# Performance work log

Measured on AMD Instinct MI355X. Metric: run time of the kernel, lower is better.

Reference implementation:

```python
import jax, jax.numpy as jnp
import numpy as np

HEAD_DIM = 64
AGGR = 4  # attn_aggr_ratio
BN_EPS = 1e-5


def _conv1x1(x, W, b=None):
    # x: [N, Cin, L], W: [Cout, Cin] -> [N, Cout, L]
    y = jnp.einsum('ncl,oc->nol', x, W)
    if b is not None:
        y = y + b[None, :, None]
    return y


def _bn(x, gamma, beta, mean, var):
    # BatchNorm1d, eval mode (running stats). x: [N, C, L]
    inv = gamma * jax.lax.rsqrt(var + BN_EPS)
    return x * inv[None, :, None] + (beta - mean * inv)[None, :, None]


def setup_inputs() -> dict:
    key = jax.random.key(0)
    ks = jax.random.split(key, 8)
    N, C, L = 4, 256, 4096
    s = 1.0 / np.sqrt(C)
    inp = {
        'x': jax.random.normal(ks[0], (N, C, L), jnp.float32),
        'Wq': jax.random.normal(ks[1], (C, C), jnp.float32) * s,
        'bq': jnp.zeros((C,), jnp.float32),
        'Wk': jax.random.normal(ks[2], (C, C), jnp.float32) * s,
        'bk': jnp.zeros((C,), jnp.float32),
        'Wv': jax.random.normal(ks[3], (C, C), jnp.float32) * s,
        'bv': jnp.zeros((C,), jnp.float32),
        'Wo': jax.random.normal(ks[4], (C, C), jnp.float32) * s,
        'bo': jnp.zeros((C,), jnp.float32),
        'Wa': jax.random.normal(ks[5], (C, C), jnp.float32) * s,
        'g1': jnp.ones((C,), jnp.float32), 'b1': jnp.zeros((C,), jnp.float32),
        'm1': jnp.zeros((C,), jnp.float32), 'v1': jnp.ones((C,), jnp.float32),
        'g2': jnp.ones((C,), jnp.float32), 'b2': jnp.zeros((C,), jnp.float32),
        'm2': jnp.zeros((C,), jnp.float32), 'v2': jnp.ones((C,), jnp.float32),
    }
    return inp


def reference(x, Wq, bq, Wk, bk, Wv, bv, Wo, bo, Wa,
              g1, b1, m1, v1, g2, b2, m2, v2):
    N, C, L = x.shape
    H, E = C // HEAD_DIM, HEAD_DIM
    # q projection on full-resolution input
    q = _conv1x1(x, Wq, bq).reshape(N, H, E, L)
    # LocalAwareAggregationBlock: avg+max pool (kernel=AGGR, L divisible), 1x1 conv, BN
    xp = x.reshape(N, C, L // AGGR, AGGR)
    xa = xp.mean(axis=-1) + xp.max(axis=-1)          # [N, C, L//AGGR]
    xa = _conv1x1(xa, Wa)                             # bias=False
    xa = _bn(xa, g1, b1, m1, v1)
    # post-aggregation norm
    xa = _bn(xa, g2, b2, m2, v2)
    k = _conv1x1(xa, Wk, bk).reshape(N, H, E, -1)     # [N, H, E, L2]
    v = _conv1x1(xa, Wv, bv).reshape(N, H, E, -1)
    # attention: softmax((q/sqrt(E))^T k) @ v^T
    scale = 1.0 / np.sqrt(E)
    scores = jnp.einsum('nhel,nhem->nhlm', q * scale, k)  # [N, H, L, L2]
    attn = jax.nn.softmax(scores, axis=-1)
    o = jnp.einsum('nhlm,nhem->nhel', attn, v).reshape(N, C, L)
    return _conv1x1(o, Wo, bo)
```

## Files before the change

### kernel.cpp

```cpp
#include <hip/hip_runtime.h>
#include <stdint.h>

constexpr int NBATCH = 4;
constexpr int CH     = 256;
constexpr int LEN    = 4096;
constexpr int LPOOL  = 1024;
constexpr int NH     = 4;
constexpr int HD     = 64;

typedef __attribute__((ext_vector_type(8))) short short8;
typedef __attribute__((ext_vector_type(4))) float float4e;

__device__ __forceinline__ unsigned short f2bf(float f) {
    union { unsigned int i; float f; } v; v.f = f;
    unsigned int lsb = (v.i >> 16) & 1u;
    v.i += 0x7fffu + lsb;
    return (unsigned short)(v.i >> 16);
}
__device__ __forceinline__ unsigned pack2bf(float lo, float hi) {
    unsigned a = __float_as_uint(lo) + 0x8000u;
    unsigned b = __float_as_uint(hi) + 0x8000u;
    return __builtin_amdgcn_perm(b, a, 0x07060302u);
}

__global__ __launch_bounds__(256) void transpool_setup(
    const float* __restrict__ x, unsigned short* __restrict__ xbf,
    unsigned short* __restrict__ poolT,
    const float* __restrict__ w0, const float* __restrict__ w1,
    const float* __restrict__ w2, const float* __restrict__ w3,
    const float* __restrict__ w4, unsigned short* __restrict__ outW,
    const float* __restrict__ g1, const float* __restrict__ b1,
    const float* __restrict__ m1, const float* __restrict__ v1,
    const float* __restrict__ g2, const float* __restrict__ b2,
    const float* __restrict__ m2, const float* __restrict__ v2,
    float* __restrict__ scale, float* __restrict__ shift,
    const float* __restrict__ bk, const float* __restrict__ bv,
    float* __restrict__ bkv)
{
    __shared__ float T[64][65];
    __shared__ float P16[64][17];
    int b = blockIdx.x, t = threadIdx.x;
    if (b >= 1024) {
        int sb = b - 1024;
        if (sb < 320) {
            int gid = sb * 256 + t;
            int w = gid >> 14;
            int off = (gid & 16383) * 4;
            const float* src = (w == 0) ? w0 : (w == 1) ? w1 : (w == 2) ? w2 : (w == 3) ? w3 : w4;
            float4 v = *(const float4*)(src + off);
            uint2 pk;
            pk.x = pack2bf(v.x, v.y);
            pk.y = pack2bf(v.z, v.w);
            *(uint2*)(outW + w * 65536 + off) = pk;
        } else {
            float inv1 = g1[t] * rsqrtf(v1[t] + 1e-5f);
            float inv2 = g2[t] * rsqrtf(v2[t] + 1e-5f);
            scale[t] = inv1 * inv2;
            shift[t] = (b1[t] - m1[t] * inv1) * inv2 + (b2[t] - m2[t] * inv2);
            bkv[t] = bk[t];
            bkv[256 + t] = bv[t];
        }
        return;
    }
    int n = b >> 8, c0 = ((b >> 6) & 3) * 64, l0 = (b & 63) * 64;
    const float* xp = x + ((size_t)n * CH + c0) * LEN + l0;
    #pragma unroll
    for (int i = 0; i < 4; i++) {
        int idx = t + i * 256;
        int c = idx >> 4, l4 = idx & 15;
        float4 v = *(const float4*)(xp + (size_t)c * LEN + l4 * 4);
        T[c][l4 * 4 + 0] = v.x; T[c][l4 * 4 + 1] = v.y;
        T[c][l4 * 4 + 2] = v.z; T[c][l4 * 4 + 3] = v.w;
        P16[c][l4] = (v.x + v.y + v.z + v.w) * 0.25f
                   + fmaxf(fmaxf(v.x, v.y), fmaxf(v.z, v.w));
    }
    __syncthreads();
    unsigned short* op = xbf + ((size_t)n * LEN + l0) * CH + c0;
    #pragma unroll
    for (int i = 0; i < 4; i++) {
        int idx = t + i * 256;
        int l = idx >> 4, c4 = idx & 15;
        uint2 pk;
        pk.x = pack2bf(T[c4 * 4 + 0][l], T[c4 * 4 + 1][l]);
        pk.y = pack2bf(T[c4 * 4 + 2][l], T[c4 * 4 + 3][l]);
        *(uint2*)(op + (size_t)l * CH + c4 * 4) = pk;
    }
    int p0 = l0 >> 2;
    #pragma unroll
    for (int k = 0; k < 2; k++) {
        int p = (t >> 5) + k * 8;
        int c2 = (t & 31) * 2;
        unsigned pk = pack2bf(P16[c2][p], P16[c2 + 1][p]);
        *(unsigned*)(poolT + ((size_t)n * LPOOL + p0 + p) * CH + c0 + c2) = pk;
    }
}

__global__ __launch_bounds__(256) void gemm_mfma(
    const unsigned short* __restrict__ A,
    const unsigned short* __restrict__ B, size_t bBatch,
    const float* __restrict__ biasRow,
    const float* __restrict__ scale, const float* __restrict__ shift,
    float* __restrict__ outF, size_t oFBatch,
    unsigned short* __restrict__ out1, size_t o1Batch, int cs1,
    unsigned short* __restrict__ out2, size_t o2Batch, int rs2, int rowSplit,
    int NN, float outScale)
{
    __shared__ unsigned short smem[2 * 128 * 72];
    unsigned short* As = smem;
    unsigned short* Bs = smem + 128 * 72;

    int n = blockIdx.z;
    int t = threadIdx.x;
    int wave = t >> 6, lane = t & 63, m = lane & 15, quad = lane >> 4;
    int wm = wave & 1, wn = wave >> 1;
    int rowTile = blockIdx.y * 128;
    int col0 = blockIdx.x * 128;

    const unsigned short* Ab = A + (size_t)rowTile * 256;
    const unsigned short* Bb = B + (size_t)n * bBatch + (size_t)col0 * 256;

    float4e acc[4][4] = {};

    for (int kk = 0; kk < 256; kk += 64) {
        #pragma unroll
        for (int i = 0; i < 4; i++) {
            int idx = t + i * 256;
            int row = idx >> 3, ch = idx & 7;
            *(uint4*)&As[row * 72 + ch * 8] = *(const uint4*)(Ab + (size_t)row * 256 + kk + ch * 8);
            *(uint4*)&Bs[row * 72 + ch * 8] = *(const uint4*)(Bb + (size_t)row * 256 + kk + ch * 8);
        }
        __syncthreads();
        #pragma unroll
        for (int kc = 0; kc < 2; kc++) {
            short8 af[4], bfr[4];
            #pragma unroll
            for (int i = 0; i < 4; i++)
                af[i] = *(const short8*)&As[(wm * 64 + i * 16 + m) * 72 + kc * 32 + quad * 8];
            #pragma unroll
            for (int j = 0; j < 4; j++)
                bfr[j] = *(const short8*)&Bs[(wn * 64 + j * 16 + m) * 72 + kc * 32 + quad * 8];
            #pragma unroll
            for (int i = 0; i < 4; i++)
                #pragma unroll
                for (int j = 0; j < 4; j++)
                    acc[i][j] = __builtin_amdgcn_mfma_f32_16x16x32_bf16(af[i], bfr[j], acc[i][j], 0, 0, 0);
        }
        __syncthreads();
    }

    if (outF) {
        float* TOf = (float*)smem;
        float* dst = outF + (size_t)n * oFBatch;
        #pragma unroll
        for (int half = 0; half < 2; half++) {
            __syncthreads();
            if (wm == half) {
                #pragma unroll
                for (int i = 0; i < 4; i++) {
                    int rowL = i * 16 + quad * 4;
                    int rowG = rowTile + half * 64 + rowL;
                    float br[4], sc[4], sh[4];
                    #pragma unroll
                    for (int r = 0; r < 4; r++) {
                        br[r] = biasRow ? biasRow[rowG + r] : 0.0f;
                        sc[r] = scale ? scale[rowG + r] : 1.0f;
                        sh[r] = shift ? shift[rowG + r] : 0.0f;
                    }
                    #pragma unroll
                    for (int j = 0; j < 4; j++) {
                        int colL = wn * 64 + j * 16 + m;
                        float4e c = acc[i][j];
                        #pragma unroll
                        for (int r = 0; r < 4; r++)
                            TOf[(rowL + r) * 128 + colL] = ((c[r] + br[r]) * sc[r] + sh[r]) * outScale;
                    }
                }
            }
            __syncthreads();
            #pragma unroll
            for (int w = 0; w < 8; w++) {
                int idx = t + w * 256;
                int row = idx >> 5, c4 = idx & 31;
                *(float4*)(dst + (size_t)(rowTile + half * 64 + row) * NN + col0 + c4 * 4) =
                    *(const float4*)&TOf[row * 128 + c4 * 4];
            }
        }
        return;
    }

    bool mode2 = (rowTile >= rowSplit);
    unsigned short* TO = smem;
    #pragma unroll
    for (int i = 0; i < 4; i++) {
        int rowL = wm * 64 + i * 16 + quad * 4;
        int rowG = rowTile + rowL;
        float br[4], sc[4], sh[4];
        #pragma unroll
        for (int r = 0; r < 4; r++) {
            br[r] = biasRow ? biasRow[rowG + r] : 0.0f;
            sc[r] = scale ? scale[rowG + r] : 1.0f;
            sh[r] = shift ? shift[rowG + r] : 0.0f;
        }
        #pragma unroll
        for (int j = 0; j < 4; j++) {
            int colL = wn * 64 + j * 16 + m;
            float4e c = acc[i][j];
            float v0 = ((c[0] + br[0]) * sc[0] + sh[0]) * outScale;
            float v1 = ((c[1] + br[1]) * sc[1] + sh[1]) * outScale;
            float v2 = ((c[2] + br[2]) * sc[2] + sh[2]) * outScale;
            float v3 = ((c[3] + br[3]) * sc[3] + sh[3]) * outScale;
            if (!mode2) {
                uint2 pk;
                pk.x = pack2bf(v0, v1);
                pk.y = pack2bf(v2, v3);
                *(uint2*)&TO[colL * 136 + rowL] = pk;
            } else {
                TO[(rowL + 0) * 136 + colL] = f2bf(v0);
                TO[(rowL + 1) * 136 + colL] = f2bf(v1);
                TO[(rowL + 2) * 136 + colL] = f2bf(v2);
                TO[(rowL + 3) * 136 + colL] = f2bf(v3);
            }
        }
    }
    __syncthreads();
    if (!mode2) {
        unsigned short* dst = out1 + (size_t)n * o1Batch;
        #pragma unroll
        for (int w = 0; w < 8; w++) {
            int idx = t + w * 256;
            int l = idx >> 4, ch = idx & 15;
            *(uint4*)(dst + (size_t)(col0 + l) * cs1 + rowTile + ch * 8) =
                *(const uint4*)&TO[l * 136 + ch * 8];
        }
    } else {
        unsigned short* dst = out2 + (size_t)n * o2Batch;
        int rowBase = rowTile - rowSplit;
        #pragma unroll
        for (int w = 0; w < 8; w++) {
            int idx = t + w * 256;
            int row = idx >> 4, ch = idx & 15;
            *(uint4*)(dst + (size_t)(rowBase + row) * rs2 + col0 + ch * 8) =
                *(const uint4*)&TO[row * 136 + ch * 8];
        }
    }
}

__global__ __launch_bounds__(256, 2) void attn_mfma(
    const unsigned short* __restrict__ Qb,
    const unsigned short* __restrict__ Kb,
    const unsigned short* __restrict__ Vb,
    unsigned short* __restrict__ Obf)
{
    __shared__ unsigned short Ks[2][128 * 72];
    __shared__ unsigned short Vs[2][64 * 136];

    int qb = blockIdx.x;
    int h  = blockIdx.y;
    int n  = blockIdx.z;
    int t  = threadIdx.x;
    int wave = t >> 6, lane = t & 63;
    int m = lane & 15, quad = lane >> 4;
    int l0 = qb * 128 + wave * 32;

    const unsigned short* qp = Qb + ((size_t)n * LEN + l0 + m) * CH + h * HD + quad * 8;
    short8 bQ[2][2];
    bQ[0][0] = *(const short8*)qp;
    bQ[0][1] = *(const short8*)(qp + 32);
    bQ[1][0] = *(const short8*)(qp + 16 * CH);
    bQ[1][1] = *(const short8*)(qp + 16 * CH + 32);

    float4e Oa[2][4] = {};
    float l_run[2] = {0.0f, 0.0f};

    const unsigned short* KgBase = Kb + (size_t)n * LPOOL * CH + h * HD;
    const unsigned short* VgBase = Vb + ((size_t)n * CH + h * HD) * LPOOL;
    const float NEG = -17.312340f;

    int krow[4], kch[4], ve[4], vch[4];
    #pragma unroll
    for (int i = 0; i < 4; i++) {
        int idx = t + i * 256;
        krow[i] = idx >> 3; kch[i] = idx & 7;
        ve[i]   = idx >> 4; vch[i] = idx & 15;
    }

    uint4 kreg[4], vreg[4];
    #pragma unroll
    for (int i = 0; i < 4; i++) {
        kreg[i] = *(const uint4*)(KgBase + (size_t)krow[i] * CH + kch[i] * 8);
        vreg[i] = *(const uint4*)(VgBase + (size_t)ve[i] * LPOOL + vch[i] * 8);
    }
    #pragma unroll
    for (int i = 0; i < 4; i++) {
        *(uint4*)&Ks[0][krow[i] * 72 + kch[i] * 8] = kreg[i];
        *(uint4*)&Vs[0][ve[i] * 136 + vch[i] * 8] = vreg[i];
    }
    __syncthreads();

    for (int kt = 0; kt < 8; kt++) {
        int cur = kt & 1;
        if (kt < 7) {
            const unsigned short* Kg2 = KgBase + (size_t)(kt + 1) * 128 * CH;
            const unsigned short* Vg2 = VgBase + (kt + 1) * 128;
            #pragma unroll
            for (int i = 0; i < 4; i++) {
                kreg[i] = *(const uint4*)(Kg2 + (size_t)krow[i] * CH + kch[i] * 8);
                vreg[i] = *(const uint4*)(Vg2 + (size_t)ve[i] * LPOOL + vch[i] * 8);
            }
        }

        #pragma unroll
        for (int ch2 = 0; ch2 < 4; ch2++) {
            const unsigned short* kpE = &Ks[cur][(ch2 * 32 + m) * 72 + quad * 8];
            const unsigned short* kpO = kpE + 16 * 72;
            short8 aE0 = *(const short8*)kpE;
            short8 aE1 = *(const short8*)(kpE + 32);
            short8 aO0 = *(const short8*)kpO;
            short8 aO1 = *(const short8*)(kpO + 32);
            union { unsigned u[4]; short8 s; } aV[4];
            #pragma unroll
            for (int eb = 0; eb < 4; eb++) {
                const unsigned short* vp = &Vs[cur][(eb * 16 + m) * 136 + ch2 * 32 + quad * 4];
                *(uint2*)&aV[eb].u[0] = *(const uint2*)vp;
                *(uint2*)&aV[eb].u[2] = *(const uint2*)(vp + 16);
            }

            #pragma unroll
            for (int qf = 0; qf < 2; qf++) {
                float4e cE = {NEG, NEG, NEG, NEG};
                cE = __builtin_amdgcn_mfma_f32_16x16x32_bf16(aE0, bQ[qf][0], cE, 0, 0, 0);
                cE = __builtin_amdgcn_mfma_f32_16x16x32_bf16(aE1, bQ[qf][1], cE, 0, 0, 0);
                float4e cO = {NEG, NEG, NEG, NEG};
                cO = __builtin_amdgcn_mfma_f32_16x16x32_bf16(aO0, bQ[qf][0], cO, 0, 0, 0);
                cO = __builtin_amdgcn_mfma_f32_16x16x32_bf16(aO1, bQ[qf][1], cO, 0, 0, 0);
                float pE0 = exp2f(cE[0]), pE1 = exp2f(cE[1]);
                float pE2 = exp2f(cE[2]), pE3 = exp2f(cE[3]);
                float pO0 = exp2f(cO[0]), pO1 = exp2f(cO[1]);
                float pO2 = exp2f(cO[2]), pO3 = exp2f(cO[3]);
                l_run[qf] += ((pE0 + pE1) + (pE2 + pE3)) + ((pO0 + pO1) + (pO2 + pO3));
                union { unsigned u[4]; short8 s; } bP;
                bP.u[0] = pack2bf(pE0, pE1);
                bP.u[1] = pack2bf(pE2, pE3);
                bP.u[2] = pack2bf(pO0, pO1);
                bP.u[3] = pack2bf(pO2, pO3);
                #pragma unroll
                for (int eb = 0; eb < 4; eb++)
                    Oa[qf][eb] = __builtin_amdgcn_mfma_f32_16x16x32_bf16(aV[eb].s, bP.s, Oa[qf][eb], 0, 0, 0);
            }
        }

        if (kt < 7) {
            int nxt = cur ^ 1;
            #pragma unroll
            for (int i = 0; i < 4; i++) {
                *(uint4*)&Ks[nxt][krow[i] * 72 + kch[i] * 8] = kreg[i];
                *(uint4*)&Vs[nxt][ve[i] * 136 + vch[i] * 8] = vreg[i];
            }
            __syncthreads();
        }
    }

    #pragma unroll
    for (int qf = 0; qf < 2; qf++) {
        float l = l_run[qf];
        l += __shfl_xor(l, 16);
        l += __shfl_xor(l, 32);
        float inv = 1.0f / l;
        unsigned short* op = Obf + ((size_t)n * LEN + l0 + qf * 16 + m) * CH + h * HD;
        #pragma unroll
        for (int eb = 0; eb < 4; eb++) {
            uint2 pk;
            pk.x = pack2bf(Oa[qf][eb][0] * inv, Oa[qf][eb][1] * inv);
            pk.y = pack2bf(Oa[qf][eb][2] * inv, Oa[qf][eb][3] * inv);
            *(uint2*)(op + eb * 16 + quad * 4) = pk;
        }
    }
}

extern "C" void kernel_launch(void* const* d_in, const int* in_sizes, int n_in,
                              void* d_out, int out_size, void* d_ws, size_t ws_size,
                              hipStream_t stream)
{
    const float* x  = (const float*)d_in[0];
    const float* Wq = (const float*)d_in[1];
    const float* bq = (const float*)d_in[2];
    const float* Wk = (const float*)d_in[3];
    const float* bk = (const float*)d_in[4];
    const float* Wv = (const float*)d_in[5];
    const float* bv = (const float*)d_in[6];
    const float* Wo = (const float*)d_in[7];
    const float* bo = (const float*)d_in[8];
    const float* Wa = (const float*)d_in[9];
    const float* g1 = (const float*)d_in[10];
    const float* b1 = (const float*)d_in[11];
    const float* m1 = (const float*)d_in[12];
    const float* v1 = (const float*)d_in[13];
    const float* g2 = (const float*)d_in[14];
    const float* b2 = (const float*)d_in[15];
    const float* m2 = (const float*)d_in[16];
    const float* v2 = (const float*)d_in[17];

    float* wsf      = (float*)d_ws;
    float* bn_scale = wsf;
    float* bn_shift = wsf + 256;
    float* bkv      = wsf + 512;
    unsigned short* Wbf   = (unsigned short*)(wsf + 1024);
    unsigned short* xbf   = Wbf + 5 * 65536;
    unsigned short* poolT = xbf   + (size_t)NBATCH * LEN * CH;
    unsigned short* xabf  = poolT + (size_t)NBATCH * LPOOL * CH;
    unsigned short* Kbf   = xabf  + (size_t)NBATCH * LPOOL * CH;
    unsigned short* Vbf   = Kbf   + (size_t)NBATCH * LPOOL * CH;
    unsigned short* Qbf   = Vbf   + (size_t)NBATCH * LPOOL * CH;
    unsigned short* Obf   = Qbf   + (size_t)NBATCH * LEN * CH;

    transpool_setup<<<1345, 256, 0, stream>>>(x, xbf, poolT,
        Wq, Wk, Wv, Wo, Wa, Wbf,
        g1, b1, m1, v1, g2, b2, m2, v2, bn_scale, bn_shift, bk, bv, bkv);

    gemm_mfma<<<dim3(32, 2, 4), 256, 0, stream>>>(
        Wbf + 0 * 65536, xbf, (size_t)LEN * CH, bq, nullptr, nullptr,
        nullptr, 0, Qbf, (size_t)LEN * CH, 256, nullptr, 0, 0, 1 << 30,
        LEN, 0.18033688f);

    gemm_mfma<<<dim3(8, 2, 4), 256, 0, stream>>>(
        Wbf + 4 * 65536, poolT, (size_t)LPOOL * CH, nullptr, bn_scale, bn_shift,
        nullptr, 0, xabf, (size_t)LPOOL * CH, 256, nullptr, 0, 0, 1 << 30,
        LPOOL, 1.0f);

    gemm_mfma<<<dim3(8, 4, 4), 256, 0, stream>>>(
        Wbf + 1 * 65536, xabf, (size_t)LPOOL * CH, bkv, nullptr, nullptr,
        nullptr, 0, Kbf, (size_t)LPOOL * CH, 256, Vbf, (size_t)LPOOL * CH, LPOOL, 256,
        LPOOL, 1.0f);

    attn_mfma<<<dim3(LEN / 128, NH, NBATCH), 256, 0, stream>>>(Qbf, Kbf, Vbf, Obf);

    gemm_mfma<<<dim3(32, 2, 4), 256, 0, stream>>>(
        Wbf + 3 * 65536, Obf, (size_t)LEN * CH, bo, nullptr, nullptr,
        (float*)d_out, (size_t)CH * LEN, nullptr, 0, 0, nullptr, 0, 0, 1 << 30,
        LEN, 1.0f);
}
```

Before: 174.9 us.

## Fold aggregation conv and BN into K/V weights, merge Q and KV GEMMs

The pooled-conv (Wa) plus the two eval-mode batchnorms are folded algebraically into combined K/V weights, Wk·diag(scale)·Wa, with a folded bias. The small weight-combining GEMMs are computed inside the setup kernel's extra blocks. This removes the intermediate xabf GEMM pass and its buffer. The Q projection and the K/V projection are merged into a single launch, cutting the launch count from five to three. The cost is extra MFMA work plus uncoalesced weight transposition in the setup kernel, and the folded weights are rounded to bf16.

```diff
diff --git a/kernel.cpp b/kernel.cpp
--- a/kernel.cpp
+++ b/kernel.cpp
@@ -33,35 +33,135 @@
     const float* __restrict__ m1, const float* __restrict__ v1,
     const float* __restrict__ g2, const float* __restrict__ b2,
     const float* __restrict__ m2, const float* __restrict__ v2,
-    float* __restrict__ scale, float* __restrict__ shift,
     const float* __restrict__ bk, const float* __restrict__ bv,
     float* __restrict__ bkv)
 {
-    __shared__ float T[64][65];
-    __shared__ float P16[64][17];
+    __shared__ union {
+        struct { float T[64][65]; float P16[64][17]; } tp;
+        struct { float scF[256]; float shF[256]; float bp[128][8];
+                 unsigned short Cs[2 * 128 * 72]; } cp;
+    } sh;
     int b = blockIdx.x, t = threadIdx.x;
+
     if (b >= 1024) {
         int sb = b - 1024;
-        if (sb < 320) {
-            int gid = sb * 256 + t;
-            int w = gid >> 14;
-            int off = (gid & 16383) * 4;
-            const float* src = (w == 0) ? w0 : (w == 1) ? w1 : (w == 2) ? w2 : (w == 3) ? w3 : w4;
+        if (sb < 128) {
+            int w = sb >> 6;
+            int off = (sb & 63) * 1024 + t * 4;
+            const float* src = (w == 0) ? w0 : w3;
+            int slot = (w == 0) ? 0 : 3;
             float4 v = *(const float4*)(src + off);
             uint2 pk;
             pk.x = pack2bf(v.x, v.y);
             pk.y = pack2bf(v.z, v.w);
-            *(uint2*)(outW + w * 65536 + off) = pk;
-        } else {
+            *(uint2*)(outW + slot * 65536 + off) = pk;
+            return;
+        }
+        int cb = sb - 128;
+        int mat = cb >> 2;
+        int tile = cb & 3;
+        int rowT = (tile >> 1) * 128, colT = (tile & 1) * 128;
+        const float* Wsrc = mat ? w2 : w1;
+        const float* bsrc = mat ? bv : bk;
+
+        {
             float inv1 = g1[t] * rsqrtf(v1[t] + 1e-5f);
             float inv2 = g2[t] * rsqrtf(v2[t] + 1e-5f);
-            scale[t] = inv1 * inv2;
-            shift[t] = (b1[t] - m1[t] * inv1) * inv2 + (b2[t] - m2[t] * inv2);
-            bkv[t] = bk[t];
-            bkv[256 + t] = bv[t];
+            sh.cp.scF[t] = inv1 * inv2;
+            sh.cp.shF[t] = (b1[t] - m1[t] * inv1) * inv2 + (b2[t] - m2[t] * inv2);
+        }
+        __syncthreads();
+
+        unsigned short* As = sh.cp.Cs;
+        unsigned short* Bs = sh.cp.Cs + 128 * 72;
+        int wave = t >> 6, lane = t & 63, m = lane & 15, quad = lane >> 4;
+        int wm = wave & 1, wn = wave >> 1;
+        float4e acc[4][4] = {};
+        float regB[4] = {};
+
+        for (int cc = 0; cc < 256; cc += 64) {
+            __syncthreads();
+            #pragma unroll
+            for (int i = 0; i < 4; i++) {
+                int idx = t + i * 256, row = idx >> 3, c8 = idx & 7;
+                const float* sp = Wsrc + (size_t)(rowT + row) * 256 + cc + c8 * 8;
+                float4 a = *(const float4*)sp, b4 = *(const float4*)(sp + 4);
+                int ci = cc + c8 * 8;
+                regB[i] += a.x * sh.cp.shF[ci]     + a.y * sh.cp.shF[ci + 1]
+                         + a.z * sh.cp.shF[ci + 2] + a.w * sh.cp.shF[ci + 3]
+                         + b4.x * sh.cp.shF[ci + 4] + b4.y * sh.cp.shF[ci + 5]
+                         + b4.z * sh.cp.shF[ci + 6] + b4.w * sh.cp.shF[ci + 7];
+                uint4 pk;
+                pk.x = pack2bf(a.x * sh.cp.scF[ci],     a.y * sh.cp.scF[ci + 1]);
+                pk.y = pack2bf(a.z * sh.cp.scF[ci + 2], a.w * sh.cp.scF[ci + 3]);
+                pk.z = pack2bf(b4.x * sh.cp.scF[ci + 4], b4.y * sh.cp.scF[ci + 5]);
+                pk.w = pack2bf(b4.z * sh.cp.scF[ci + 6], b4.w * sh.cp.scF[ci + 7]);
+                *(uint4*)&As[row * 72 + c8 * 8] = pk;
+            }
+            #pragma unroll
+            for (int i = 0; i < 8; i++) {
+                int idx = t + i * 256, c = idx >> 5, j4 = (idx & 31) * 4;
+                float4 w = *(const float4*)(w4 + (size_t)(cc + c) * 256 + colT + j4);
+                Bs[(j4 + 0) * 72 + c] = f2bf(w.x);
+                Bs[(j4 + 1) * 72 + c] = f2bf(w.y);
+                Bs[(j4 + 2) * 72 + c] = f2bf(w.z);
+                Bs[(j4 + 3) * 72 + c] = f2bf(w.w);
+            }
+            __syncthreads();
+            #pragma unroll
+            for (int kc = 0; kc < 2; kc++) {
+                short8 af[4], bfr[4];
+                #pragma unroll
+                for (int i = 0; i < 4; i++)
+                    af[i] = *(const short8*)&As[(wm * 64 + i * 16 + m) * 72 + kc * 32 + quad * 8];
+                #pragma unroll
+                for (int j = 0; j < 4; j++)
+                    bfr[j] = *(const short8*)&Bs[(wn * 64 + j * 16 + m) * 72 + kc * 32 + quad * 8];
+                #pragma unroll
+                for (int i = 0; i < 4; i++)
+                    #pragma unroll
+                    for (int j = 0; j < 4; j++)
+                        acc[i][j] = __builtin_amdgcn_mfma_f32_16x16x32_bf16(af[i], bfr[j], acc[i][j], 0, 0, 0);
+            }
+        }
+        __syncthreads();
+        if (colT == 0) {
+            #pragma unroll
+            for (int i = 0; i < 4; i++) {
+                int idx = t + i * 256;
+                sh.cp.bp[idx >> 3][idx & 7] = regB[i];
+            }
+        }
+        unsigned short* TO = sh.cp.Cs;
+        #pragma unroll
+        for (int i = 0; i < 4; i++) {
+            int rowL = wm * 64 + i * 16 + quad * 4;
+            #pragma unroll
+            for (int j = 0; j < 4; j++) {
+                int colL = wn * 64 + j * 16 + m;
+                float4e c = acc[i][j];
+                TO[(rowL + 0) * 136 + colL] = f2bf(c[0]);
+                TO[(rowL + 1) * 136 + colL] = f2bf(c[1]);
+                TO[(rowL + 2) * 136 + colL] = f2bf(c[2]);
+                TO[(rowL + 3) * 136 + colL] = f2bf(c[3]);
+            }
+        }
+        __syncthreads();
+        #pragma unroll
+        for (int w = 0; w < 8; w++) {
+            int idx = t + w * 256, row = idx >> 4, ch = idx & 15;
+            *(uint4*)(outW + 65536 + (size_t)(mat * 256 + rowT + row) * 256 + colT + ch * 8) =
+                *(const uint4*)&TO[row * 136 + ch * 8];
+        }
+        if (colT == 0 && t < 128) {
+            float s = bsrc[rowT + t];
+            #pragma unroll
+            for (int u = 0; u < 8; u++) s += sh.cp.bp[t][u];
+            bkv[mat * 256 + rowT + t] = s;
         }
         return;
     }
+
     int n = b >> 8, c0 = ((b >> 6) & 3) * 64, l0 = (b & 63) * 64;
     const float* xp = x + ((size_t)n * CH + c0) * LEN + l0;
     #pragma unroll
@@ -69,10 +169,10 @@
         int idx = t + i * 256;
         int c = idx >> 4, l4 = idx & 15;
         float4 v = *(const float4*)(xp + (size_t)c * LEN + l4 * 4);
-        T[c][l4 * 4 + 0] = v.x; T[c][l4 * 4 + 1] = v.y;
-        T[c][l4 * 4 + 2] = v.z; T[c][l4 * 4 + 3] = v.w;
-        P16[c][l4] = (v.x + v.y + v.z + v.w) * 0.25f
-                   + fmaxf(fmaxf(v.x, v.y), fmaxf(v.z, v.w));
+        sh.tp.T[c][l4 * 4 + 0] = v.x; sh.tp.T[c][l4 * 4 + 1] = v.y;
+        sh.tp.T[c][l4 * 4 + 2] = v.z; sh.tp.T[c][l4 * 4 + 3] = v.w;
+        sh.tp.P16[c][l4] = (v.x + v.y + v.z + v.w) * 0.25f
+                         + fmaxf(fmaxf(v.x, v.y), fmaxf(v.z, v.w));
     }
     __syncthreads();
     unsigned short* op = xbf + ((size_t)n * LEN + l0) * CH + c0;
@@ -81,8 +181,8 @@
         int idx = t + i * 256;
         int l = idx >> 4, c4 = idx & 15;
         uint2 pk;
-        pk.x = pack2bf(T[c4 * 4 + 0][l], T[c4 * 4 + 1][l]);
-        pk.y = pack2bf(T[c4 * 4 + 2][l], T[c4 * 4 + 3][l]);
+        pk.x = pack2bf(sh.tp.T[c4 * 4 + 0][l], sh.tp.T[c4 * 4 + 1][l]);
+        pk.y = pack2bf(sh.tp.T[c4 * 4 + 2][l], sh.tp.T[c4 * 4 + 3][l]);
         *(uint2*)(op + (size_t)l * CH + c4 * 4) = pk;
     }
     int p0 = l0 >> 2;
@@ -90,34 +190,26 @@
     for (int k = 0; k < 2; k++) {
         int p = (t >> 5) + k * 8;
         int c2 = (t & 31) * 2;
-        unsigned pk = pack2bf(P16[c2][p], P16[c2 + 1][p]);
+        unsigned pk = pack2bf(sh.tp.P16[c2][p], sh.tp.P16[c2 + 1][p]);
         *(unsigned*)(poolT + ((size_t)n * LPOOL + p0 + p) * CH + c0 + c2) = pk;
     }
 }
 
-__global__ __launch_bounds__(256) void gemm_mfma(
-    const unsigned short* __restrict__ A,
-    const unsigned short* __restrict__ B, size_t bBatch,
+__device__ __forceinline__ void gemm_body(
+    const unsigned short* __restrict__ Ab,
+    const unsigned short* __restrict__ Bb,
+    int rowTile, int col0,
     const float* __restrict__ biasRow,
-    const float* __restrict__ scale, const float* __restrict__ shift,
-    float* __restrict__ outF, size_t oFBatch,
-    unsigned short* __restrict__ out1, size_t o1Batch, int cs1,
-    unsigned short* __restrict__ out2, size_t o2Batch, int rs2, int rowSplit,
-    int NN, float outScale)
+    float* __restrict__ outF, int NN,
+    unsigned short* __restrict__ out1, int cs1,
+    unsigned short* __restrict__ out2, int rs2, int rowSplit,
+    float outScale, unsigned short* smem)
 {
-    __shared__ unsigned short smem[2 * 128 * 72];
     unsigned short* As = smem;
     unsigned short* Bs = smem + 128 * 72;
-
-    int n = blockIdx.z;
     int t = threadIdx.x;
     int wave = t >> 6, lane = t & 63, m = lane & 15, quad = lane >> 4;
     int wm = wave & 1, wn = wave >> 1;
-    int rowTile = blockIdx.y * 128;
-    int col0 = blockIdx.x * 128;
-
-    const unsigned short* Ab = A + (size_t)rowTile * 256;
-    const unsigned short* Bb = B + (size_t)n * bBatch + (size_t)col0 * 256;
 
     float4e acc[4][4] = {};
 
@@ -150,7 +242,6 @@
 
     if (outF) {
         float* TOf = (float*)smem;
-        float* dst = outF + (size_t)n * oFBatch;
         #pragma unroll
         for (int half = 0; half < 2; half++) {
             __syncthreads();
@@ -159,20 +250,17 @@
                 for (int i = 0; i < 4; i++) {
                     int rowL = i * 16 + quad * 4;
                     int rowG = rowTile + half * 64 + rowL;
-                    float br[4], sc[4], sh[4];
+                    float br[4];
                     #pragma unroll
-                    for (int r = 0; r < 4; r++) {
+                    for (int r = 0; r < 4; r++)
                         br[r] = biasRow ? biasRow[rowG + r] : 0.0f;
-                        sc[r] = scale ? scale[rowG + r] : 1.0f;
-                        sh[r] = shift ? shift[rowG + r] : 0.0f;
-                    }
                     #pragma unroll
                     for (int j = 0; j < 4; j++) {
                         int colL = wn * 64 + j * 16 + m;
                         float4e c = acc[i][j];
                         #pragma unroll
                         for (int r = 0; r < 4; r++)
-                            TOf[(rowL + r) * 128 + colL] = ((c[r] + br[r]) * sc[r] + sh[r]) * outScale;
+                            TOf[(rowL + r) * 128 + colL] = (c[r] + br[r]) * outScale;
                     }
                 }
             }
@@ -181,7 +269,7 @@
             for (int w = 0; w < 8; w++) {
                 int idx = t + w * 256;
                 int row = idx >> 5, c4 = idx & 31;
-                *(float4*)(dst + (size_t)(rowTile + half * 64 + row) * NN + col0 + c4 * 4) =
+                *(float4*)(outF + (size_t)(rowTile + half * 64 + row) * NN + col0 + c4 * 4) =
                     *(const float4*)&TOf[row * 128 + c4 * 4];
             }
         }
@@ -194,21 +282,18 @@
     for (int i = 0; i < 4; i++) {
         int rowL = wm * 64 + i * 16 + quad * 4;
         int rowG = rowTile + rowL;
-        float br[4], sc[4], sh[4];
-        #pragma unroll
-        for (int r = 0; r < 4; r++) {
+        float br[4];
+        #pragma unroll
+        for (int r = 0; r < 4; r++)
             br[r] = biasRow ? biasRow[rowG + r] : 0.0f;
-            sc[r] = scale ? scale[rowG + r] : 1.0f;
-            sh[r] = shift ? shift[rowG + r] : 0.0f;
-        }
         #pragma unroll
         for (int j = 0; j < 4; j++) {
             int colL = wn * 64 + j * 16 + m;
             float4e c = acc[i][j];
-            float v0 = ((c[0] + br[0]) * sc[0] + sh[0]) * outScale;
-            float v1 = ((c[1] + br[1]) * sc[1] + sh[1]) * outScale;
-            float v2 = ((c[2] + br[2]) * sc[2] + sh[2]) * outScale;
-            float v3 = ((c[3] + br[3]) * sc[3] + sh[3]) * outScale;
+            float v0 = (c[0] + br[0]) * outScale;
+            float v1 = (c[1] + br[1]) * outScale;
+            float v2 = (c[2] + br[2]) * outScale;
+            float v3 = (c[3] + br[3]) * outScale;
             if (!mode2) {
                 uint2 pk;
                 pk.x = pack2bf(v0, v1);
@@ -224,25 +309,72 @@
     }
     __syncthreads();
     if (!mode2) {
-        unsigned short* dst = out1 + (size_t)n * o1Batch;
         #pragma unroll
         for (int w = 0; w < 8; w++) {
             int idx = t + w * 256;
             int l = idx >> 4, ch = idx & 15;
-            *(uint4*)(dst + (size_t)(col0 + l) * cs1 + rowTile + ch * 8) =
+            *(uint4*)(out1 + (size_t)(col0 + l) * cs1 + rowTile + ch * 8) =
                 *(const uint4*)&TO[l * 136 + ch * 8];
         }
     } else {
-        unsigned short* dst = out2 + (size_t)n * o2Batch;
         int rowBase = rowTile - rowSplit;
         #pragma unroll
         for (int w = 0; w < 8; w++) {
             int idx = t + w * 256;
             int row = idx >> 4, ch = idx & 15;
-            *(uint4*)(dst + (size_t)(rowBase + row) * rs2 + col0 + ch * 8) =
+            *(uint4*)(out2 + (size_t)(rowBase + row) * rs2 + col0 + ch * 8) =
                 *(const uint4*)&TO[row * 136 + ch * 8];
         }
     }
+}
+
+__global__ __launch_bounds__(256) void gemm_qkv(
+    const unsigned short* __restrict__ Wbf,
+    const unsigned short* __restrict__ xbf,
+    const unsigned short* __restrict__ poolT,
+    const float* __restrict__ bq, const float* __restrict__ bkv,
+    unsigned short* __restrict__ Qbf,
+    unsigned short* __restrict__ Kbf,
+    unsigned short* __restrict__ Vbf)
+{
+    __shared__ unsigned short smem[2 * 128 * 72];
+    int n = blockIdx.z, bx = blockIdx.x;
+    if (bx < 64) {
+        int colT = (bx & 31) * 128, rowT = (bx >> 5) * 128;
+        gemm_body(Wbf + (size_t)rowT * 256,
+                  xbf + (size_t)n * LEN * CH + (size_t)colT * 256,
+                  rowT, colT, bq,
+                  nullptr, 0,
+                  Qbf + (size_t)n * LEN * CH, 256,
+                  nullptr, 0, 1 << 30,
+                  0.18033688f, smem);
+    } else {
+        int j = bx - 64;
+        int colT = (j & 7) * 128, rowT = (j >> 3) * 128;
+        gemm_body(Wbf + 65536 + (size_t)rowT * 256,
+                  poolT + (size_t)n * LPOOL * CH + (size_t)colT * 256,
+                  rowT, colT, bkv,
+                  nullptr, 0,
+                  Kbf + (size_t)n * LPOOL * CH, 256,
+                  Vbf + (size_t)n * LPOOL * CH, LPOOL, 256,
+                  1.0f, smem);
+    }
+}
+
+__global__ __launch_bounds__(256) void gemm_o(
+    const unsigned short* __restrict__ Wbf3,
+    const unsigned short* __restrict__ Obf,
+    const float* __restrict__ bo, float* __restrict__ out)
+{
+    __shared__ unsigned short smem[2 * 128 * 72];
+    int n = blockIdx.z;
+    int colT = blockIdx.x * 128, rowT = blockIdx.y * 128;
+    gemm_body(Wbf3 + (size_t)rowT * 256,
+              Obf + (size_t)n * LEN * CH + (size_t)colT * 256,
+              rowT, colT, bo,
+              out + (size_t)n * CH * LEN, LEN,
+              nullptr, 0, nullptr, 0, 1 << 30,
+              1.0f, smem);
 }
 
 __global__ __launch_bounds__(256, 2) void attn_mfma(
@@ -400,42 +532,25 @@
     const float* m2 = (const float*)d_in[16];
     const float* v2 = (const float*)d_in[17];
 
-    float* wsf      = (float*)d_ws;
-    float* bn_scale = wsf;
-    float* bn_shift = wsf + 256;
-    float* bkv      = wsf + 512;
-    unsigned short* Wbf   = (unsigned short*)(wsf + 1024);
+    float* wsf = (float*)d_ws;
+    float* bkv = wsf;
+    unsigned short* Wbf   = (unsigned short*)(wsf + 512);
     unsigned short* xbf   = Wbf + 5 * 65536;
     unsigned short* poolT = xbf   + (size_t)NBATCH * LEN * CH;
-    unsigned short* xabf  = poolT + (size_t)NBATCH * LPOOL * CH;
-    unsigned short* Kbf   = xabf  + (size_t)NBATCH * LPOOL * CH;
+    unsigned short* Kbf   = poolT + (size_t)NBATCH * LPOOL * CH;
     unsigned short* Vbf   = Kbf   + (size_t)NBATCH * LPOOL * CH;
     unsigned short* Qbf   = Vbf   + (size_t)NBATCH * LPOOL * CH;
     unsigned short* Obf   = Qbf   + (size_t)NBATCH * LEN * CH;
 
-    transpool_setup<<<1345, 256, 0, stream>>>(x, xbf, poolT,
+    transpool_setup<<<1160, 256, 0, stream>>>(x, xbf, poolT,
         Wq, Wk, Wv, Wo, Wa, Wbf,
-        g1, b1, m1, v1, g2, b2, m2, v2, bn_scale, bn_shift, bk, bv, bkv);
-
-    gemm_mfma<<<dim3(32, 2, 4), 256, 0, stream>>>(
-        Wbf + 0 * 65536, xbf, (size_t)LEN * CH, bq, nullptr, nullptr,
-        nullptr, 0, Qbf, (size_t)LEN * CH, 256, nullptr, 0, 0, 1 << 30,
-        LEN, 0.18033688f);
-
-    gemm_mfma<<<dim3(8, 2, 4), 256, 0, stream>>>(
-        Wbf + 4 * 65536, poolT, (size_t)LPOOL * CH, nullptr, bn_scale, bn_shift,
-        nullptr, 0, xabf, (size_t)LPOOL * CH, 256, nullptr, 0, 0, 1 << 30,
-        LPOOL, 1.0f);
-
-    gemm_mfma<<<dim3(8, 4, 4), 256, 0, stream>>>(
-        Wbf + 1 * 65536, xabf, (size_t)LPOOL * CH, bkv, nullptr, nullptr,
-        nullptr, 0, Kbf, (size_t)LPOOL * CH, 256, Vbf, (size_t)LPOOL * CH, LPOOL, 256,
-        LPOOL, 1.0f);
+        g1, b1, m1, v1, g2, b2, m2, v2, bk, bv, bkv);
+
+    gemm_qkv<<<dim3(96, 1, 4), 256, 0, stream>>>(
+        Wbf, xbf, poolT, bq, bkv, Qbf, Kbf, Vbf);
 
     attn_mfma<<<dim3(LEN / 128, NH, NBATCH), 256, 0, stream>>>(Qbf, Kbf, Vbf, Obf);
 
-    gemm_mfma<<<dim3(32, 2, 4), 256, 0, stream>>>(
-        Wbf + 3 * 65536, Obf, (size_t)LEN * CH, bo, nullptr, nullptr,
-        (float*)d_out, (size_t)CH * LEN, nullptr, 0, 0, nullptr, 0, 0, 1 << 30,
-        LEN, 1.0f);
-}
+    gemm_o<<<dim3(32, 2, 4), 256, 0, stream>>>(
+        Wbf + 3 * 65536, Obf, bo, (float*)d_out);
+}
```

Result: no change. 178.2 us (+1.9%).
